# Kernel tuning notes

Hardware: AMD Instinct MI355X
Metric: run time of the kernel (lower is better)

## Reference

```python
import jax, jax.numpy as jnp
import numpy as np

K = 3
PAD = 1


def conv3x3(x, w, b):
    # x: [B,Ci,H,W], w: [Co,Ci,3,3] -> [B,Co,H,W]
    y = jax.lax.conv_general_dilated(
        x, w, window_strides=(1, 1), padding=((PAD, PAD), (PAD, PAD)),
        dimension_numbers=('NCHW', 'OIHW', 'NCHW'))
    return y + b[None, :, None, None]


def _gather(x_flat, idx):
    # x_flat: [C, H*W], idx: [K2*H*W] -> [C, K2*H*W]
    return x_flat[:, idx]


def deform_sample(x, off_x, off_y, mask):
    """Modulated deformable im2col (DCNv2, dg=1, stride=1, pad=1, dil=1).
    x: [B,C,H,W]; off_x, off_y, mask: [B,K2,H,W] -> cols [B,C,K2,H,W]."""
    B, C, H, W = x.shape
    K2 = K * K
    # static kernel-tap displacements relative to output pixel
    dy = jnp.repeat(jnp.arange(K), K) - PAD          # [K2]
    dx = jnp.tile(jnp.arange(K), K) - PAD            # [K2]
    gy = jnp.arange(H)[:, None].astype(x.dtype)      # [H,1]
    gx = jnp.arange(W)[None, :].astype(x.dtype)      # [1,W]
    ys = gy[None, None] + dy[None, :, None, None].astype(x.dtype) + off_y  # [B,K2,H,W]
    xs = gx[None, None] + dx[None, :, None, None].astype(x.dtype) + off_x
    y0 = jnp.floor(ys)
    x0 = jnp.floor(xs)
    wy1 = ys - y0
    wx1 = xs - x0
    xf = x.reshape(B, C, H * W)
    val = jnp.zeros((B, C, K2, H, W), x.dtype)
    for oy, ox in ((0, 0), (0, 1), (1, 0), (1, 1)):
        yy = y0 + oy
        xx = x0 + ox
        wgt = (wy1 if oy else 1.0 - wy1) * (wx1 if ox else 1.0 - wx1)
        valid = ((yy >= 0) & (yy < H) & (xx >= 0) & (xx < W)).astype(x.dtype)
        idx = (jnp.clip(yy, 0, H - 1) * W + jnp.clip(xx, 0, W - 1)).astype(jnp.int32)
        g = jax.vmap(_gather)(xf, idx.reshape(B, -1)).reshape(B, C, K2, H, W)
        val = val + (wgt * valid)[:, None] * g
    return val * mask[:, None]  # modulation, broadcast over C


def reference(x, feat, w_off, b_off, w_def, b_def):
    # offset/mask prediction conv (3*K2 channels), chunked as in the torch module
    om = conv3x3(feat, w_off, b_off)
    off_x, off_y, m = jnp.split(om, 3, axis=1)   # each [B,K2,H,W]
    mask = jax.nn.sigmoid(m)
    cols = deform_sample(x, off_x, off_y, mask)  # [B,C,K2,H,W]
    O = w_def.shape[0]
    out = jnp.einsum('bckhw,ock->bohw', cols, w_def.reshape(O, -1, K * K))
    out = out + b_def[None, :, None, None]
    return jax.nn.relu(out)


def setup_inputs() -> dict:
    key = jax.random.key(0)
    k1, k2, k3, k4 = jax.random.split(key, 4)
    B, C, O, H, W = 4, 64, 64, 128, 128
    K2 = K * K
    x = jax.random.normal(k1, (B, C, H, W), jnp.float32)
    feat = jax.random.normal(k2, (B, C, H, W), jnp.float32)
    # offset conv params: small init so offsets stay near zero (as in practice)
    w_off = jax.random.normal(k3, (3 * K2, C, 3, 3), jnp.float32) * 0.01
    b_off = jnp.zeros((3 * K2,), jnp.float32)
    w_def = jax.random.normal(k4, (O, C, 3, 3), jnp.float32) * (1.0 / np.sqrt(C * K2))
    b_def = jnp.zeros((O,), jnp.float32)
    return {"x": x, "feat": feat, "w_off": w_off, "b_off": b_off,
            "w_def": w_def, "b_def": b_def}
```

## Files before the change

kernel.cpp:

```cpp
#include <hip/hip_runtime.h>
#include <math.h>

#define Bn 4
#define Cn 64
#define On 64
#define Hn 128
#define Wn 128
#define HWn (Hn * Wn)

typedef __attribute__((ext_vector_type(8))) short s16x8;
typedef __attribute__((ext_vector_type(4))) float f32x4;

__device__ __forceinline__ unsigned short f2bf(float f) {
    unsigned u = __float_as_uint(f);
    u += 0x7fffu + ((u >> 16) & 1u);
    return (unsigned short)(u >> 16);
}
__device__ __forceinline__ float bf2f(unsigned short u) {
    return __uint_as_float(((unsigned)u) << 16);
}
__device__ __forceinline__ int swz(int row, int ch) {
    return row * 32 + (((ch ^ (row >> 1)) & 3) << 3);
}

__global__ __launch_bounds__(256) void transpose_all(const float* __restrict__ x,
                                                     const float* __restrict__ feat,
                                                     const float* __restrict__ wdef,
                                                     const float* __restrict__ woff,
                                                     ushort* __restrict__ xt,
                                                     ushort* __restrict__ ft,
                                                     ushort* __restrict__ wdT2,
                                                     ushort* __restrict__ woT2) {
    int t = threadIdx.x;
    if (blockIdx.z == 2) {
        int id = (blockIdx.y * gridDim.x + blockIdx.x) * 256 + t;
        if (id < 36864) {
            int c2 = id & 31, oc = (id >> 5) & 63, ks = id >> 11;
            int k = ks % 9, s = ks / 9;
            wdT2[id] = f2bf(wdef[(oc * 64 + s * 32 + c2) * 9 + k]);
        } else if (id < 55296) {
            int i2 = id - 36864;
            int c2 = i2 & 31, oc = (i2 >> 5) & 31, ks = i2 >> 10;
            int k = ks % 9, s = ks / 9;
            woT2[i2] = (oc < 27) ? f2bf(woff[(oc * 64 + s * 32 + c2) * 9 + k]) : (ushort)0;
        }
        return;
    }
    __shared__ float tile[64][65];
    const float* src = blockIdx.z ? feat : x;
    ushort* dst0 = blockIdx.z ? ft : xt;
    int b = blockIdx.y, hw0 = blockIdx.x * 64;
    int lane = t & 63, grp = t >> 6;
    const float* xb = src + (size_t)b * Cn * HWn;
#pragma unroll
    for (int i = 0; i < 16; ++i) {
        int c = grp * 16 + i;
        tile[lane][c] = xb[(size_t)c * HWn + hw0 + lane];
    }
    __syncthreads();
#pragma unroll
    for (int jj = 0; jj < 2; ++jj) {
        int px = jj * 32 + (t >> 3), ch = t & 7;
        s16x8 p;
#pragma unroll
        for (int j = 0; j < 8; ++j) p[j] = (short)f2bf(tile[px][ch * 8 + j]);
        *(s16x8*)(dst0 + ((size_t)(b * HWn + hw0 + px)) * Cn + ch * 8) = p;
    }
}

__global__ __launch_bounds__(256, 3) void off_conv_kernel(const ushort* __restrict__ ft,
                                                          const ushort* __restrict__ woT2,
                                                          const float* __restrict__ b_off,
                                                          float* __restrict__ om) {
    __shared__ __align__(16) char smem[43776];
    ushort* s_win = (ushort*)smem;
    ushort* s_wgt = (ushort*)(smem + 25344);
    float* s_out = (float*)smem;

    int t = threadIdx.x;
    int wv = t >> 6, l = t & 63;
    int q = l >> 4, r = l & 15;
    int h = blockIdx.x, b = blockIdx.y;
    const ushort* ft_b = ft + (size_t)b * HWn * Cn;

    f32x4 zero = {0.f, 0.f, 0.f, 0.f};
    s16x8 zz = {0, 0, 0, 0, 0, 0, 0, 0};
    f32x4 acc[2][2];
    acc[0][0] = zero; acc[0][1] = zero; acc[1][0] = zero; acc[1][1] = zero;

    for (int s = 0; s < 2; ++s) {
        for (int j = t; j < 1560; j += 256) {
            int row = j / 520, rm = j - row * 520;
            int col = rm >> 2, ch = rm & 3;
            int rs = min(max(h - 1 + row, 0), Hn - 1);
            int cs = min(max(col - 1, 0), Wn - 1);
            s16x8 v = *(const s16x8*)(ft_b + (size_t)(rs * Wn + cs) * Cn + s * 32 + ch * 8);
            *(s16x8*)&s_win[swz(row * 132 + col, ch)] = v;
        }
        for (int j = t; j < 1152; j += 256) {
            int ro = j >> 2, ch = j & 3;
            s16x8 v = *(const s16x8*)(woT2 + (size_t)s * 9216 + ro * 32 + ch * 8);
            *(s16x8*)&s_wgt[swz(ro, ch)] = v;
        }
        __syncthreads();
#pragma unroll 3
        for (int k = 0; k < 9; ++k) {
            int dy = k / 3 - 1, dx = k % 3 - 1;
            int y = h + dy;
            bool yv = (y >= 0) && (y < Hn);
#pragma unroll
            for (int mt = 0; mt < 2; ++mt) {
                int px = wv * 32 + mt * 16 + r;
                int xx = px + dx;
                bool valid = yv && (xx >= 0) && (xx < Wn);
                int lin = (dy + 1) * 132 + px + dx + 1;
                s16x8 av = *(const s16x8*)&s_win[swz(lin, q)];
                av = valid ? av : zz;
#pragma unroll
                for (int ot = 0; ot < 2; ++ot) {
                    s16x8 bv = *(const s16x8*)&s_wgt[swz(k * 32 + ot * 16 + r, q)];
                    acc[mt][ot] = __builtin_amdgcn_mfma_f32_16x16x32_bf16(av, bv, acc[mt][ot], 0, 0, 0);
                }
            }
        }
        __syncthreads();
    }
#pragma unroll
    for (int mt = 0; mt < 2; ++mt)
#pragma unroll
        for (int ot = 0; ot < 2; ++ot) {
            int oc = ot * 16 + r;
            float bo = (oc < 27) ? b_off[oc] : 0.f;
#pragma unroll
            for (int reg = 0; reg < 4; ++reg) {
                int px = wv * 32 + mt * 16 + q * 4 + reg;
                float v = acc[mt][ot][reg] + bo;
                if (oc >= 18 && oc < 27) v = 1.f / (1.f + __expf(-v));
                s_out[oc * 132 + px] = v;
            }
        }
    __syncthreads();
    for (int idx = t; idx < 27 * 128; idx += 256) {
        int o = idx >> 7, px = idx & 127;
        om[((size_t)b * 27 + o) * HWn + h * Wn + px] = s_out[o * 132 + px];
    }
}

__global__ __launch_bounds__(256, 3) void mega_kernel(const ushort* __restrict__ xt,
                                                      const ushort* __restrict__ wdT2,
                                                      const float* __restrict__ om,
                                                      const float* __restrict__ b_def,
                                                      float* __restrict__ out) {
    __shared__ __align__(16) char smem[42272];
    ushort* s_win = (ushort*)smem;
    ushort* s_wgt = (ushort*)(smem + 21760);
    int* s_flag = (int*)(smem + 42240);
    float* s_om = (float*)(smem + 21760);
    float* s_out = (float*)smem;

    int t = threadIdx.x;
    int wv = t >> 6, l = t & 63;
    int q = l >> 4, r = l & 15;
    int p0 = blockIdx.x * 64;
    int b = p0 >> 14;
    int rem = p0 & (HWn - 1);
    int h = rem >> 7;
    int wbase = rem & (Wn - 1);
    int pxi = wv * 16 + r;
    float pxif = (float)pxi;
    const ushort* xt_b = xt + (size_t)b * HWn * Cn;

    for (int j = t; j < 1728; j += 256) {
        int o = j >> 6, px = j & 63;
        s_om[o * 68 + px] = om[((size_t)b * 27 + o) * HWn + h * Wn + wbase + px];
    }
    __syncthreads();
    float omv[27];
#pragma unroll
    for (int o = 0; o < 27; ++o) omv[o] = s_om[o * 68 + pxi];
    bool okp = true;
#pragma unroll
    for (int k = 0; k < 9; ++k) {
        float uy = (float)(k / 3 - 1) + omv[9 + k];
        float ux = pxif + (float)(k % 3 - 1) + omv[k];
        okp = okp && (uy >= -2.f) && (uy < 2.f) && (ux >= -2.f) && (ux < 65.f);
    }
    int allok = __all(okp) ? 1 : 0;
    if (l == 0) s_flag[wv] = allok;
    __syncthreads();
    int fast = s_flag[0] & s_flag[1] & s_flag[2] & s_flag[3];

    f32x4 zero = {0.f, 0.f, 0.f, 0.f};
    f32x4 acc[4];
    acc[0] = zero; acc[1] = zero; acc[2] = zero; acc[3] = zero;

    if (fast) {
        auto tap = [&](int k, int krel) {
            float uy = (float)(k / 3 - 1) + omv[9 + k];
            float ux = pxif + (float)(k % 3 - 1) + omv[k];
            float mv = omv[18 + k];
            float y0f = floorf(uy), x0f = floorf(ux);
            float fy = uy - y0f, fx = ux - x0f;
            int iy = (int)y0f + 2;
            int ix = (int)x0f + 2;
            int yab = h + (int)y0f, xab = wbase + (int)x0f;
            bool vy0 = (yab >= 0) && (yab < Hn);
            bool vy1 = (yab + 1 >= 0) && (yab + 1 < Hn);
            bool vx0 = (xab >= 0) && (xab < Wn);
            bool vx1 = (xab + 1 >= 0) && (xab + 1 < Wn);
            float g0 = (vy0 && vx0) ? (1.f - fy) * (1.f - fx) * mv : 0.f;
            float g1 = (vy0 && vx1) ? (1.f - fy) * fx * mv : 0.f;
            float g2 = (vy1 && vx0) ? fy * (1.f - fx) * mv : 0.f;
            float g3 = (vy1 && vx1) ? fy * fx * mv : 0.f;
            int lin0 = iy * 68 + ix;
            s16x8 q0 = *(const s16x8*)&s_win[swz(lin0, q)];
            s16x8 q1 = *(const s16x8*)&s_win[swz(lin0 + 1, q)];
            s16x8 q2 = *(const s16x8*)&s_win[swz(lin0 + 68, q)];
            s16x8 q3 = *(const s16x8*)&s_win[swz(lin0 + 69, q)];
            s16x8 af;
#pragma unroll
            for (int j = 0; j < 8; ++j) {
                float rr = g0 * bf2f((unsigned short)q0[j]) + g1 * bf2f((unsigned short)q1[j])
                         + g2 * bf2f((unsigned short)q2[j]) + g3 * bf2f((unsigned short)q3[j]);
                af[j] = (short)f2bf(rr);
            }
#pragma unroll
            for (int ot = 0; ot < 4; ++ot) {
                s16x8 bv = *(const s16x8*)&s_wgt[swz(krel * 64 + ot * 16 + r, q)];
                acc[ot] = __builtin_amdgcn_mfma_f32_16x16x32_bf16(af, bv, acc[ot], 0, 0, 0);
            }
        };

        for (int s = 0; s < 2; ++s) {
            for (int j = t; j < 1360; j += 256) {
                int row = j / 272, rm = j - row * 272;
                int col = rm >> 2, ch = rm & 3;
                int rs = min(max(h - 2 + row, 0), Hn - 1);
                int cs = min(max(wbase - 2 + col, 0), Wn - 1);
                s16x8 v = *(const s16x8*)(xt_b + (size_t)(rs * Wn + cs) * Cn + s * 32 + ch * 8);
                *(s16x8*)&s_win[swz(row * 68 + col, ch)] = v;
            }
            for (int j = t; j < 1280; j += 256) {
                int ro = j >> 2, ch = j & 3;
                s16x8 v = *(const s16x8*)(wdT2 + (size_t)s * 18432 + ro * 32 + ch * 8);
                *(s16x8*)&s_wgt[swz(ro, ch)] = v;
            }
            __syncthreads();
#pragma unroll 5
            for (int k = 0; k < 5; ++k) tap(k, k);
            __syncthreads();
            for (int j = t; j < 1024; j += 256) {
                int ro = j >> 2, ch = j & 3;
                s16x8 v = *(const s16x8*)(wdT2 + (size_t)s * 18432 + (320 + ro) * 32 + ch * 8);
                *(s16x8*)&s_wgt[swz(ro, ch)] = v;
            }
            __syncthreads();
#pragma unroll 4
            for (int k = 5; k < 9; ++k) tap(k, k - 5);
            __syncthreads();
        }
    } else {
#pragma unroll 1
        for (int k = 0; k < 9; ++k) {
            float ys = (float)(h + k / 3 - 1) + omv[9 + k];
            float xs = (float)(wbase + pxi + k % 3 - 1) + omv[k];
            float mv = omv[18 + k];
            float y0f = floorf(ys), x0f = floorf(xs);
            float fy = ys - y0f, fx = xs - x0f;
            int y0 = (int)y0f, x0 = (int)x0f;
            float g[4];
            int a[4];
#pragma unroll
            for (int n = 0; n < 4; ++n) {
                int yy = y0 + (n >> 1), xx = x0 + (n & 1);
                bool valid = (yy >= 0) && (yy < Hn) && (xx >= 0) && (xx < Wn);
                float wgt = ((n >> 1) ? fy : 1.f - fy) * ((n & 1) ? fx : 1.f - fx) * mv;
                g[n] = valid ? wgt : 0.f;
                int yc = min(max(yy, 0), Hn - 1), xc = min(max(xx, 0), Wn - 1);
                a[n] = (yc * Wn + xc) * Cn;
            }
#pragma unroll
            for (int s = 0; s < 2; ++s) {
                int c = s * 32 + q * 8;
                s16x8 q0 = *(const s16x8*)(xt_b + a[0] + c);
                s16x8 q1 = *(const s16x8*)(xt_b + a[1] + c);
                s16x8 q2 = *(const s16x8*)(xt_b + a[2] + c);
                s16x8 q3 = *(const s16x8*)(xt_b + a[3] + c);
                s16x8 af;
#pragma unroll
                for (int j = 0; j < 8; ++j) {
                    float rr = g[0] * bf2f((unsigned short)q0[j]) + g[1] * bf2f((unsigned short)q1[j])
                             + g[2] * bf2f((unsigned short)q2[j]) + g[3] * bf2f((unsigned short)q3[j]);
                    af[j] = (short)f2bf(rr);
                }
#pragma unroll
                for (int ot = 0; ot < 4; ++ot) {
                    s16x8 bv = *(const s16x8*)(wdT2 + (size_t)s * 18432
                                               + (size_t)(k * 64 + ot * 16 + r) * 32 + q * 8);
                    acc[ot] = __builtin_amdgcn_mfma_f32_16x16x32_bf16(af, bv, acc[ot], 0, 0, 0);
                }
            }
        }
    }
    __syncthreads();

#pragma unroll
    for (int ot = 0; ot < 4; ++ot) {
        int oc = ot * 16 + r;
        float bv = b_def[oc];
        f32x4 vv;
#pragma unroll
        for (int reg = 0; reg < 4; ++reg) vv[reg] = fmaxf(acc[ot][reg] + bv, 0.f);
        *(f32x4*)&s_out[oc * 68 + wv * 16 + q * 4] = vv;
    }
    __syncthreads();
    {
        int px = t & 63, og = t >> 6;
        float* ob = out + ((size_t)b * On) * HWn + h * Wn + wbase;
#pragma unroll
        for (int j = 0; j < 16; ++j) {
            int oc = og * 16 + j;
            ob[(size_t)oc * HWn + px] = s_out[oc * 68 + px];
        }
    }
}

extern "C" void kernel_launch(void* const* d_in, const int* in_sizes, int n_in,
                              void* d_out, int out_size, void* d_ws, size_t ws_size,
                              hipStream_t stream) {
    const float* x = (const float*)d_in[0];
    const float* feat = (const float*)d_in[1];
    const float* w_off = (const float*)d_in[2];
    const float* b_off = (const float*)d_in[3];
    const float* w_def = (const float*)d_in[4];
    const float* b_def = (const float*)d_in[5];
    float* out = (float*)d_out;

    char* ws = (char*)d_ws;
    ushort* xt = (ushort*)ws;
    ushort* ft = (ushort*)(ws + 8388608);
    ushort* wdT2 = (ushort*)(ws + 16777216);
    ushort* woT2 = (ushort*)(ws + 16850944);
    float* om = (float*)(ws + 16887808);

    hipLaunchKernelGGL(transpose_all, dim3(HWn / 64, Bn, 3), dim3(256), 0, stream,
                       x, feat, w_def, w_off, xt, ft, wdT2, woT2);
    hipLaunchKernelGGL(off_conv_kernel, dim3(Hn, Bn), dim3(256), 0, stream,
                       ft, woT2, b_off, om);
    hipLaunchKernelGGL(mega_kernel, dim3((Bn * HWn) / 64), dim3(256), 0, stream,
                       xt, wdT2, om, b_def, out);
}
```

Before: 148.0 us.

## Stage full 64-channel window once and read deform weights directly from global

```diff
diff --git a/kernel.cpp b/kernel.cpp
--- a/kernel.cpp
+++ b/kernel.cpp
@@ -151,17 +151,17 @@
                                                       const float* __restrict__ om,
                                                       const float* __restrict__ b_def,
                                                       float* __restrict__ out) {
-    __shared__ __align__(16) char smem[42272];
+    __shared__ __align__(16) char smem[43536];
     ushort* s_win = (ushort*)smem;
-    ushort* s_wgt = (ushort*)(smem + 21760);
-    int* s_flag = (int*)(smem + 42240);
-    float* s_om = (float*)(smem + 21760);
+    int* s_flag = (int*)(smem + 43520);
+    float* s_om = (float*)smem;
     float* s_out = (float*)smem;
 
     int t = threadIdx.x;
     int wv = t >> 6, l = t & 63;
     int q = l >> 4, r = l & 15;
-    int p0 = blockIdx.x * 64;
+    int blk = (blockIdx.x & 7) * 128 + (blockIdx.x >> 3);
+    int p0 = blk * 64;
     int b = p0 >> 14;
     int rem = p0 & (HWn - 1);
     int h = rem >> 7;
@@ -172,12 +172,12 @@
 
     for (int j = t; j < 1728; j += 256) {
         int o = j >> 6, px = j & 63;
-        s_om[o * 68 + px] = om[((size_t)b * 27 + o) * HWn + h * Wn + wbase + px];
+        s_om[o * 64 + px] = om[((size_t)b * 27 + o) * HWn + h * Wn + wbase + px];
     }
     __syncthreads();
     float omv[27];
 #pragma unroll
-    for (int o = 0; o < 27; ++o) omv[o] = s_om[o * 68 + pxi];
+    for (int o = 0; o < 27; ++o) omv[o] = s_om[o * 64 + pxi];
     bool okp = true;
 #pragma unroll
     for (int k = 0; k < 9; ++k) {
@@ -190,12 +190,23 @@
     __syncthreads();
     int fast = s_flag[0] & s_flag[1] & s_flag[2] & s_flag[3];
 
+    for (int j = t; j < 2720; j += 256) {
+        int lin = j >> 3, cidx = j & 7;
+        int row = lin / 68, col = lin - row * 68;
+        int rs = min(max(h - 2 + row, 0), Hn - 1);
+        int cs = min(max(wbase - 2 + col, 0), Wn - 1);
+        s16x8 v = *(const s16x8*)(xt_b + (size_t)(rs * Wn + cs) * Cn + cidx * 8);
+        *(s16x8*)&s_win[lin * 64 + (((cidx + lin) & 7) << 3)] = v;
+    }
+    __syncthreads();
+
     f32x4 zero = {0.f, 0.f, 0.f, 0.f};
     f32x4 acc[4];
     acc[0] = zero; acc[1] = zero; acc[2] = zero; acc[3] = zero;
 
     if (fast) {
-        auto tap = [&](int k, int krel) {
+#pragma unroll 3
+        for (int k = 0; k < 9; ++k) {
             float uy = (float)(k / 3 - 1) + omv[9 + k];
             float ux = pxif + (float)(k % 3 - 1) + omv[k];
             float mv = omv[18 + k];
@@ -212,52 +223,36 @@
             float g1 = (vy0 && vx1) ? (1.f - fy) * fx * mv : 0.f;
             float g2 = (vy1 && vx0) ? fy * (1.f - fx) * mv : 0.f;
             float g3 = (vy1 && vx1) ? fy * fx * mv : 0.f;
-            int lin0 = iy * 68 + ix;
-            s16x8 q0 = *(const s16x8*)&s_win[swz(lin0, q)];
-            s16x8 q1 = *(const s16x8*)&s_win[swz(lin0 + 1, q)];
-            s16x8 q2 = *(const s16x8*)&s_win[swz(lin0 + 68, q)];
-            s16x8 q3 = *(const s16x8*)&s_win[swz(lin0 + 69, q)];
-            s16x8 af;
-#pragma unroll
-            for (int j = 0; j < 8; ++j) {
-                float rr = g0 * bf2f((unsigned short)q0[j]) + g1 * bf2f((unsigned short)q1[j])
-                         + g2 * bf2f((unsigned short)q2[j]) + g3 * bf2f((unsigned short)q3[j]);
-                af[j] = (short)f2bf(rr);
-            }
-#pragma unroll
-            for (int ot = 0; ot < 4; ++ot) {
-                s16x8 bv = *(const s16x8*)&s_wgt[swz(krel * 64 + ot * 16 + r, q)];
-                acc[ot] = __builtin_amdgcn_mfma_f32_16x16x32_bf16(af, bv, acc[ot], 0, 0, 0);
-            }
-        };
-
-        for (int s = 0; s < 2; ++s) {
-            for (int j = t; j < 1360; j += 256) {
-                int row = j / 272, rm = j - row * 272;
-                int col = rm >> 2, ch = rm & 3;
-                int rs = min(max(h - 2 + row, 0), Hn - 1);
-                int cs = min(max(wbase - 2 + col, 0), Wn - 1);
-                s16x8 v = *(const s16x8*)(xt_b + (size_t)(rs * Wn + cs) * Cn + s * 32 + ch * 8);
-                *(s16x8*)&s_win[swz(row * 68 + col, ch)] = v;
-            }
-            for (int j = t; j < 1280; j += 256) {
-                int ro = j >> 2, ch = j & 3;
-                s16x8 v = *(const s16x8*)(wdT2 + (size_t)s * 18432 + ro * 32 + ch * 8);
-                *(s16x8*)&s_wgt[swz(ro, ch)] = v;
-            }
-            __syncthreads();
-#pragma unroll 5
-            for (int k = 0; k < 5; ++k) tap(k, k);
-            __syncthreads();
-            for (int j = t; j < 1024; j += 256) {
-                int ro = j >> 2, ch = j & 3;
-                s16x8 v = *(const s16x8*)(wdT2 + (size_t)s * 18432 + (320 + ro) * 32 + ch * 8);
-                *(s16x8*)&s_wgt[swz(ro, ch)] = v;
-            }
-            __syncthreads();
-#pragma unroll 4
-            for (int k = 5; k < 9; ++k) tap(k, k - 5);
-            __syncthreads();
+            int l0 = iy * 68 + ix, l1 = l0 + 1, l2 = l0 + 68, l3 = l0 + 69;
+            s16x8 bw[2][4];
+#pragma unroll
+            for (int s = 0; s < 2; ++s)
+#pragma unroll
+                for (int ot = 0; ot < 4; ++ot)
+                    bw[s][ot] = *(const s16x8*)(wdT2 + (size_t)s * 18432
+                                                + (size_t)(k * 64 + ot * 16 + r) * 32 + q * 8);
+            s16x8 af[2];
+#pragma unroll
+            for (int s = 0; s < 2; ++s) {
+                int c = s * 4 + q;
+                s16x8 q0 = *(const s16x8*)&s_win[l0 * 64 + (((c + l0) & 7) << 3)];
+                s16x8 q1 = *(const s16x8*)&s_win[l1 * 64 + (((c + l1) & 7) << 3)];
+                s16x8 q2 = *(const s16x8*)&s_win[l2 * 64 + (((c + l2) & 7) << 3)];
+                s16x8 q3 = *(const s16x8*)&s_win[l3 * 64 + (((c + l3) & 7) << 3)];
+                s16x8 p;
+#pragma unroll
+                for (int j = 0; j < 8; ++j) {
+                    float rr = g0 * bf2f((unsigned short)q0[j]) + g1 * bf2f((unsigned short)q1[j])
+                             + g2 * bf2f((unsigned short)q2[j]) + g3 * bf2f((unsigned short)q3[j]);
+                    p[j] = (short)f2bf(rr);
+                }
+                af[s] = p;
+            }
+#pragma unroll
+            for (int s = 0; s < 2; ++s)
+#pragma unroll
+                for (int ot = 0; ot < 4; ++ot)
+                    acc[ot] = __builtin_amdgcn_mfma_f32_16x16x32_bf16(af[s], bw[s][ot], acc[ot], 0, 0, 0);
         }
     } else {
 #pragma unroll 1
```

New measurement: 140.3 us. 1.05x faster.
